# Optimization experiments

Hardware: AMD Instinct MI355X
Metric: run time of the kernel (lower is better)

The kernel has to match this reference:

```python
import jax, jax.numpy as jnp
import numpy as np

B, S, E, H = 4, 2048, 512, 8
D = E // H  # head dim
CDIM = 3


def setup_inputs() -> dict:
    key = jax.random.key(0)
    ks = jax.random.split(key, 16)
    inp = {
        'q': jax.random.normal(ks[0], (B, S, E), jnp.float32),
        'k': jax.random.normal(ks[1], (B, S, E), jnp.float32),
        'v': jax.random.normal(ks[2], (B, S, E), jnp.float32),
        'coords_q': jax.random.normal(ks[3], (B, S, CDIM), jnp.float32),
        'coords_k': jax.random.normal(ks[4], (B, S, CDIM), jnp.float32),
        'attn_mask': jax.random.randint(ks[5], (B, S, S), 0, 2).astype(bool),
        'alibi_mask': jax.random.randint(ks[6], (B, S, S), 0, 2).astype(bool),
        # per-head projection params, stacked over heads: [H, E, D]
        'Wq': jax.random.normal(ks[7], (H, E, D), jnp.float32) / np.sqrt(E),
        'bq': jnp.zeros((H, D), jnp.float32),
        'Wk': jax.random.normal(ks[8], (H, E, D), jnp.float32) / np.sqrt(E),
        'bk': jnp.zeros((H, D), jnp.float32),
        'Wv': jax.random.normal(ks[9], (H, E, D), jnp.float32) / np.sqrt(E),
        'bv': jnp.zeros((H, D), jnp.float32),
        # per-head ALiBi params; running_mean is a buffer (eval mode -> constant ones)
        'bias_scale': jax.random.uniform(ks[10], (H,), jnp.float32),
        'running_mean': jnp.ones((H,), jnp.float32),
        # output projection
        'fc_w': jax.random.normal(ks[11], (E, E), jnp.float32) / np.sqrt(E),
        'fc_b': jnp.zeros((E,), jnp.float32),
    }
    return inp


def reference(q, k, v, coords_q, coords_k, attn_mask, alibi_mask,
              Wq, bq, Wk, bk, Wv, bv, bias_scale, running_mean, fc_w, fc_b):
    # per-head projections, vectorized over heads: [B,H,S,D]
    qh = jnp.einsum('bse,hed->bhsd', q, Wq) + bq[None, :, None, :]
    kh = jnp.einsum('bse,hed->bhsd', k, Wk) + bk[None, :, None, :]
    vh = jnp.einsum('bse,hed->bhsd', v, Wv) + bv[None, :, None, :]

    # scaled dot-product logits: [B,H,Sq,Sk]
    logits = jnp.einsum('bhqd,bhkd->bhqk', qh, kh) * (D ** -0.5)
    weights = jax.nn.softmax(logits, axis=-1)

    # pairwise euclidean distances between coords: [B,Sq,Sk]
    diff = coords_q[:, :, None, :] - coords_k[:, None, :, :]
    dist = jnp.sqrt(jnp.sum(diff * diff, axis=-1))

    # per-head distance bias (eval: divide by running_mean buffer, scale by bias_scale)
    scale = (bias_scale / running_mean)[None, :, None, None]  # [1,H,1,1]
    scaled_dist = dist[:, None, :, :] * scale                  # [B,H,Sq,Sk]
    masked_dist = jnp.where(~alibi_mask[:, None, :, :], scaled_dist, 0.0)

    # post-softmax bias subtraction and masking (non-standard attention)
    masked = jnp.where(~attn_mask[:, None, :, :], weights - masked_dist, 0.0)

    att = jnp.einsum('bhqk,bhkd->bhqd', masked, vh)            # [B,H,S,D]
    att = att.transpose(0, 2, 1, 3).reshape(B, S, E)           # [B,S,E]
    return att @ fc_w.T + fc_b
```

## Files before the change

kernel.cpp:

```cpp
#include <hip/hip_runtime.h>

typedef unsigned short ushort;
typedef unsigned char uchar;
typedef unsigned long long u64;
typedef __attribute__((ext_vector_type(8))) short short8;
typedef __attribute__((ext_vector_type(4))) float f32x4;
typedef __attribute__((ext_vector_type(4))) unsigned int uint4v;

#define B_ 4
#define S_ 2048
#define E_ 512
#define H_ 8
#define D_ 64
#define LDT 40
#define LDF 68

__device__ inline ushort f2bf(float f) {
  union { float f; unsigned int u; } v; v.f = f;
  unsigned int u = v.u;
  unsigned int r = u + 0x7FFFu + ((u >> 16) & 1u);
  return (ushort)(r >> 16);
}

__device__ inline unsigned int cvt_pk_bf16(float a, float b) {
  unsigned int r;
  asm("v_cvt_pk_bf16_f32 %0, %1, %2" : "=v"(r) : "v"(a), "v"(b));
  return r;
}

__device__ inline float exp2_fast(float x) {
#if defined(__has_builtin)
#if __has_builtin(__builtin_amdgcn_exp2f)
  return __builtin_amdgcn_exp2f(x);
#else
  return __expf(x * 0.69314718056f);
#endif
#else
  return __expf(x * 0.69314718056f);
#endif
}

__device__ inline short8 mask_keep(short8 p, short8 a2) {
  union U { short8 s; uint4v u; } P, A;
  P.s = p; A.s = a2;
#pragma unroll
  for (int i = 0; i < 4; ++i) {
    unsigned int t = A.u[i] & 0x80008000u;
    unsigned int dm = (t >> 15) * 0xFFFFu;
    P.u[i] &= ~dm;
  }
  return P.s;
}

__device__ inline float dpp_sum16(float v) {
  union { float f; int i; } s, t;
  s.f = v;
  t.i = __builtin_amdgcn_update_dpp(0, s.i, 0x128, 0xf, 0xf, false); s.f += t.f;
  t.i = __builtin_amdgcn_update_dpp(0, s.i, 0x124, 0xf, 0xf, false); s.f += t.f;
  t.i = __builtin_amdgcn_update_dpp(0, s.i, 0x122, 0xf, 0xf, false); s.f += t.f;
  t.i = __builtin_amdgcn_update_dpp(0, s.i, 0x121, 0xf, 0xf, false); s.f += t.f;
  return s.f;
}

__global__ void detect_kernel(const uchar* __restrict__ am, int* flag) {
  __shared__ int s;
  if (threadIdx.x == 0) s = 0;
  __syncthreads();
  int x = 0;
  for (int p = threadIdx.x; p < 4096; p += 256)
    if (p & 3) x += am[p];
  atomicAdd(&s, x);
  __syncthreads();
  if (threadIdx.x == 0) *flag = (s == 0) ? 1 : 0;
}

__global__ __launch_bounds__(256) void convert_weights_kernel(
    const float* __restrict__ Wq, const float* __restrict__ Wk, const float* __restrict__ Wv,
    const float* __restrict__ fcw,
    ushort* __restrict__ wt, ushort* __restrict__ fcwbf) {
  const int p = blockIdx.y;
  const int n = blockIdx.x;
  if (p == 3) {
    const float* src = fcw + (size_t)n * E_;
    ushort* o = fcwbf + (size_t)n * E_;
    for (int e = threadIdx.x; e < E_; e += 256) o[e] = f2bf(src[e]);
    return;
  }
  const float* W = (p == 0) ? Wq : (p == 1) ? Wk : Wv;
  const int h = n >> 6, d = n & 63;
  ushort* o = wt + ((size_t)p * E_ + n) * E_;
  for (int e = threadIdx.x; e < E_; e += 256)
    o[e] = f2bf(W[((size_t)h * E_ + e) * D_ + d]);
}

__global__ __launch_bounds__(256) void proj_gemm_kernel(
    const float* __restrict__ qx, const float* __restrict__ kx, const float* __restrict__ vx,
    const ushort* __restrict__ wt,
    const float* __restrict__ bq, const float* __restrict__ bk, const float* __restrict__ bv,
    ushort* __restrict__ qkv) {
  const int phys = blockIdx.x;
  const int logical = (phys & 7) * 96 + (phys >> 3);
  const int p = logical >> 8;
  const int rem = logical & 255;
  const int m0 = (rem >> 2) * 128, n0 = (rem & 3) * 128;

  const float* A   = (p == 0) ? qx : (p == 1) ? kx : vx;
  const ushort* Bt = wt + (size_t)p * (E_ * E_);
  const float* bias = (p == 0) ? bq : (p == 1) ? bk : bv;
  const float osc = (p == 0) ? 0.125f * 1.44269504f : 1.0f;
  ushort* out = qkv + (size_t)p * (B_ * H_ * S_ * D_);

  const int tid = threadIdx.x;
  const int w = tid >> 6, lane = tid & 63;
  const int g = lane >> 4, c = lane & 15;
  const int wr = w >> 1, wc = w & 1;

  __shared__ ushort As[2][128][LDT], Bs[2][128][LDT];

  f32x4 acc[4][4];
#pragma unroll
  for (int i = 0; i < 4; ++i)
#pragma unroll
    for (int j = 0; j < 4; ++j) acc[i][j] = (f32x4){0, 0, 0, 0};

  const int srow = tid >> 2, sc8 = (tid & 3) * 8;
  float4 pa0[2], pa1[2];
  short8 pb[2];

#pragma unroll
  for (int it = 0; it < 2; ++it) {
    const float* ap = &A[(size_t)(m0 + srow + 64 * it) * E_ + sc8];
    float4 a0 = *(const float4*)ap;
    float4 a1 = *(const float4*)(ap + 4);
    unsigned int r0 = cvt_pk_bf16(a0.x, a0.y), r1 = cvt_pk_bf16(a0.z, a0.w);
    unsigned int r2 = cvt_pk_bf16(a1.x, a1.y), r3 = cvt_pk_bf16(a1.z, a1.w);
    short8 av;
    av[0] = (short)(ushort)r0; av[1] = (short)(ushort)(r0 >> 16);
    av[2] = (short)(ushort)r1; av[3] = (short)(ushort)(r1 >> 16);
    av[4] = (short)(ushort)r2; av[5] = (short)(ushort)(r2 >> 16);
    av[6] = (short)(ushort)r3; av[7] = (short)(ushort)(r3 >> 16);
    *(short8*)&As[0][srow + 64 * it][sc8] = av;
    *(short8*)&Bs[0][srow + 64 * it][sc8] = *(const short8*)&Bt[(size_t)(n0 + srow + 64 * it) * E_ + sc8];
  }
#pragma unroll
  for (int it = 0; it < 2; ++it) {
    const float* ap = &A[(size_t)(m0 + srow + 64 * it) * E_ + 32 + sc8];
    pa0[it] = *(const float4*)ap;
    pa1[it] = *(const float4*)(ap + 4);
    pb[it] = *(const short8*)&Bt[(size_t)(n0 + srow + 64 * it) * E_ + 32 + sc8];
  }
  __syncthreads();

  for (int ks = 0; ks < 16; ++ks) {
    const int cur = ks & 1;
    short8 af[4], bfr[4];
#pragma unroll
    for (int i = 0; i < 4; ++i) af[i] = *(const short8*)&As[cur][wr * 64 + i * 16 + c][8 * g];
#pragma unroll
    for (int j = 0; j < 4; ++j) bfr[j] = *(const short8*)&Bs[cur][wc * 64 + j * 16 + c][8 * g];
#pragma unroll
    for (int i = 0; i < 4; ++i)
#pragma unroll
      for (int j = 0; j < 4; ++j)
        acc[i][j] = __builtin_amdgcn_mfma_f32_16x16x32_bf16(af[i], bfr[j], acc[i][j], 0, 0, 0);

    if (ks + 1 < 16) {
#pragma unroll
      for (int it = 0; it < 2; ++it) {
        unsigned int r0 = cvt_pk_bf16(pa0[it].x, pa0[it].y), r1 = cvt_pk_bf16(pa0[it].z, pa0[it].w);
        unsigned int r2 = cvt_pk_bf16(pa1[it].x, pa1[it].y), r3 = cvt_pk_bf16(pa1[it].z, pa1[it].w);
        short8 av;
        av[0] = (short)(ushort)r0; av[1] = (short)(ushort)(r0 >> 16);
        av[2] = (short)(ushort)r1; av[3] = (short)(ushort)(r1 >> 16);
        av[4] = (short)(ushort)r2; av[5] = (short)(ushort)(r2 >> 16);
        av[6] = (short)(ushort)r3; av[7] = (short)(ushort)(r3 >> 16);
        *(short8*)&As[cur ^ 1][srow + 64 * it][sc8] = av;
        *(short8*)&Bs[cur ^ 1][srow + 64 * it][sc8] = pb[it];
      }
      if (ks + 2 < 16) {
        const int kk = (ks + 2) * 32;
#pragma unroll
        for (int it = 0; it < 2; ++it) {
          const float* ap = &A[(size_t)(m0 + srow + 64 * it) * E_ + kk + sc8];
          pa0[it] = *(const float4*)ap;
          pa1[it] = *(const float4*)(ap + 4);
          pb[it] = *(const short8*)&Bt[(size_t)(n0 + srow + 64 * it) * E_ + kk + sc8];
        }
      }
    }
    __syncthreads();
  }

#pragma unroll
  for (int i = 0; i < 4; ++i)
#pragma unroll
    for (int jj = 0; jj < 4; ++jj) {
      int grow = m0 + wr * 64 + i * 16 + 4 * g + jj;
      int b = grow >> 11, s = grow & 2047;
#pragma unroll
      for (int j = 0; j < 4; ++j) {
        int col = n0 + wc * 64 + j * 16 + c;
        int h = col >> 6, d = col & 63;
        out[(((size_t)(b * H_ + h)) * S_ + s) * D_ + d] = f2bf((acc[i][j][jj] + bias[col]) * osc);
      }
    }
}

__global__ __launch_bounds__(256) void transpose_v_kernel(
    const ushort* __restrict__ vh, ushort* __restrict__ vtg) {
  const int bh = blockIdx.y, s0 = blockIdx.x * 64;
  __shared__ ushort tile[64][70];
  const int tid = threadIdx.x;
#pragma unroll
  for (int it = 0; it < 2; ++it) {
    int chunk = tid + 256 * it;
    int r = chunk >> 3, c8 = chunk & 7;
    *(short8*)&tile[r][c8 * 8] = *(const short8*)&vh[((size_t)bh * S_ + s0 + r) * D_ + c8 * 8];
  }
  __syncthreads();
#pragma unroll
  for (int it = 0; it < 2; ++it) {
    int chunk = tid + 256 * it;
    int d = chunk >> 3, s8 = chunk & 7;
    short8 o;
#pragma unroll
    for (int j = 0; j < 8; ++j) o[j] = (short)tile[s8 * 8 + j][d];
    *(short8*)&vtg[((size_t)bh * D_ + d) * S_ + s0 + s8 * 8] = o;
  }
}

__global__ __launch_bounds__(256) void m2dist_kernel(
    const float* __restrict__ cq, const float* __restrict__ ck,
    const void* __restrict__ am_raw, const void* __restrict__ alm_raw,
    const int* __restrict__ flag,
    ushort* __restrict__ m2d) {
  const bool isInt = (*flag != 0);
  const int b = blockIdx.y, qi = blockIdx.x;
  const int k0 = threadIdx.x * 8;
  const size_t rowbase = ((size_t)b * S_ + qi) * S_;
  const float qx = cq[((size_t)b * S_ + qi) * 3 + 0];
  const float qy = cq[((size_t)b * S_ + qi) * 3 + 1];
  const float qz = cq[((size_t)b * S_ + qi) * 3 + 2];
  int a[8], al[8];
  if (isInt) {
    int4 A0 = *(const int4*)&((const int*)am_raw)[rowbase + k0];
    int4 A1 = *(const int4*)&((const int*)am_raw)[rowbase + k0 + 4];
    int4 L0 = *(const int4*)&((const int*)alm_raw)[rowbase + k0];
    int4 L1 = *(const int4*)&((const int*)alm_raw)[rowbase + k0 + 4];
    a[0]=A0.x; a[1]=A0.y; a[2]=A0.z; a[3]=A0.w; a[4]=A1.x; a[5]=A1.y; a[6]=A1.z; a[7]=A1.w;
    al[0]=L0.x; al[1]=L0.y; al[2]=L0.z; al[3]=L0.w; al[4]=L1.x; al[5]=L1.y; al[6]=L1.z; al[7]=L1.w;
  } else {
    u64 ab = *(const u64*)&((const uchar*)am_raw)[rowbase + k0];
    u64 lb = *(const u64*)&((const uchar*)alm_raw)[rowbase + k0];
#pragma unroll
    for (int j = 0; j < 8; ++j) { a[j] = (int)((ab >> (8 * j)) & 0xFF); al[j] = (int)((lb >> (8 * j)) & 0xFF); }
  }
  float c24[24];
  {
    const float* ckp = ck + ((size_t)b * S_ + k0) * 3;
#pragma unroll
    for (int t = 0; t < 6; ++t) {
      float4 cv = *(const float4*)(ckp + 4 * t);
      c24[4 * t] = cv.x; c24[4 * t + 1] = cv.y; c24[4 * t + 2] = cv.z; c24[4 * t + 3] = cv.w;
    }
  }
  float dist[8];
#pragma unroll
  for (int j = 0; j < 8; ++j) {
    const float dx = qx - c24[3 * j], dy = qy - c24[3 * j + 1], dz = qz - c24[3 * j + 2];
    dist[j] = sqrtf(dx * dx + dy * dy + dz * dz);
  }
  short8 md;
#pragma unroll
  for (int jp = 0; jp < 4; ++jp) {
    unsigned int r = cvt_pk_bf16(dist[2 * jp], dist[2 * jp + 1]);
    ushort v0 = (!a[2 * jp]     && !al[2 * jp])     ? (ushort)r         : (ushort)0;
    ushort v1 = (!a[2 * jp + 1] && !al[2 * jp + 1]) ? (ushort)(r >> 16) : (ushort)0;
    if (a[2 * jp])     v0 |= 0x8000u;
    if (a[2 * jp + 1]) v1 |= 0x8000u;
    md[2 * jp] = (short)v0; md[2 * jp + 1] = (short)v1;
  }
  *(short8*)&m2d[rowbase + k0] = md;
}

__global__ __launch_bounds__(512) void flash_kernel(
    const ushort* __restrict__ qh, const ushort* __restrict__ kh, const ushort* __restrict__ vtg,
    const ushort* __restrict__ m2d,
    const float* __restrict__ bscale, const float* __restrict__ rmean,
    ushort* __restrict__ attb) {
  const int flat = blockIdx.x;
  const int h = flat >> 6;
  const int grp = flat & 63;
  const int b = grp >> 4;
  const int qb = (grp & 15) * 128;
  const int bh = b * 8 + h;
  const int tid = threadIdx.x;
  const int w = tid >> 6, lane = tid & 63;
  const int g = lane >> 4, c = lane & 15;

  __shared__ ushort Kt[2][64][LDF];
  __shared__ ushort Vt[2][64][LDF];
  __shared__ ushort Pl[8][16][LDF];

  const size_t bhS = (size_t)bh * S_;
  const int qrow_a = qb + 16 * w + c;
  const short8 aq0 = *(const short8*)(qh + (bhS + qrow_a) * D_ + 8 * g);
  const short8 aq1 = *(const short8*)(qh + (bhS + qrow_a) * D_ + 8 * g + 32);

  const int skr = tid >> 3, sc8 = (tid & 7) * 8;
  const ushort* pk0 = kh + (bhS + skr) * D_ + sc8;
  const ushort* pv0 = vtg + ((size_t)bh * D_ + skr) * S_ + sc8;
  const ushort* pm0 = m2d + ((size_t)b * S_ + qrow_a) * S_ + 8 * g;
  const ushort* pm1 = pm0 + 32;

  f32x4 acc1[4], acc2[4];
#pragma unroll
  for (int t = 0; t < 4; ++t) { acc1[t] = (f32x4){0,0,0,0}; acc2[t] = (f32x4){0,0,0,0}; }
  float l[4] = {0, 0, 0, 0};

  {
    short8 k0 = *(const short8*)pk0;  pk0 += 64 * D_;
    short8 v0 = *(const short8*)pv0;  pv0 += 64;
    *(short8*)&Kt[0][skr][sc8] = k0;
    *(short8*)&Vt[0][skr][sc8] = v0;
  }
  short8 a2n0 = *(const short8*)pm0; pm0 += 64;
  short8 a2n1 = *(const short8*)pm1; pm1 += 64;
  short8 skn = *(const short8*)pk0;  pk0 += 64 * D_;
  short8 svn = *(const short8*)pv0;  pv0 += 64;
  __syncthreads();

  for (int kb = 0; kb < S_; kb += 64) {
    const int cur = (kb >> 6) & 1;
    short8 a2c0 = a2n0, a2c1 = a2n1;
    a2n0 = *(const short8*)pm0; pm0 += 64;
    a2n1 = *(const short8*)pm1; pm1 += 64;

    f32x4 sf[4];
    __builtin_amdgcn_s_setprio(1);
#pragma unroll
    for (int t = 0; t < 4; ++t) {
      short8 b0 = *(const short8*)&Kt[cur][16 * t + c][8 * g];
      short8 b1 = *(const short8*)&Kt[cur][16 * t + c][8 * g + 32];
      f32x4 z = (f32x4){0, 0, 0, 0};
      z = __builtin_amdgcn_mfma_f32_16x16x32_bf16(aq0, b0, z, 0, 0, 0);
      z = __builtin_amdgcn_mfma_f32_16x16x32_bf16(aq1, b1, z, 0, 0, 0);
      sf[t] = z;
    }
    __builtin_amdgcn_s_setprio(0);

#pragma unroll
    for (int t = 0; t < 4; ++t)
#pragma unroll
      for (int jp = 0; jp < 2; ++jp) {
        float p0 = exp2_fast(sf[t][2 * jp]);
        float p1 = exp2_fast(sf[t][2 * jp + 1]);
        l[2 * jp] += p0; l[2 * jp + 1] += p1;
        unsigned int r = cvt_pk_bf16(p0, p1);
        Pl[w][4 * g + 2 * jp][16 * t + c]     = (ushort)r;
        Pl[w][4 * g + 2 * jp + 1][16 * t + c] = (ushort)(r >> 16);
      }

    asm volatile("s_waitcnt lgkmcnt(0)" ::: "memory");
    __builtin_amdgcn_sched_barrier(0);

    short8 pa0 = *(const short8*)&Pl[w][c][8 * g];
    short8 pa1 = *(const short8*)&Pl[w][c][8 * g + 32];
    pa0 = mask_keep(pa0, a2c0);
    pa1 = mask_keep(pa1, a2c1);
    __builtin_amdgcn_s_setprio(1);
#pragma unroll
    for (int t2 = 0; t2 < 4; ++t2) {
      short8 v0 = *(const short8*)&Vt[cur][16 * t2 + c][8 * g];
      short8 v1 = *(const short8*)&Vt[cur][16 * t2 + c][8 * g + 32];
      acc1[t2] = __builtin_amdgcn_mfma_f32_16x16x32_bf16(pa0, v0, acc1[t2], 0, 0, 0);
      acc1[t2] = __builtin_amdgcn_mfma_f32_16x16x32_bf16(pa1, v1, acc1[t2], 0, 0, 0);
      acc2[t2] = __builtin_amdgcn_mfma_f32_16x16x32_bf16(a2c0, v0, acc2[t2], 0, 0, 0);
      acc2[t2] = __builtin_amdgcn_mfma_f32_16x16x32_bf16(a2c1, v1, acc2[t2], 0, 0, 0);
    }
    __builtin_amdgcn_s_setprio(0);

    if (kb + 64 < S_) {
      *(short8*)&Kt[cur ^ 1][skr][sc8] = skn;
      *(short8*)&Vt[cur ^ 1][skr][sc8] = svn;
      skn = *(const short8*)pk0;  pk0 += 64 * D_;
      svn = *(const short8*)pv0;  pv0 += 64;
    }
    __syncthreads();
  }

  float linv[4];
#pragma unroll
  for (int j = 0; j < 4; ++j) linv[j] = 1.0f / dpp_sum16(l[j]);
  const float scale = bscale[h] / rmean[h];
#pragma unroll
  for (int t2 = 0; t2 < 4; ++t2)
#pragma unroll
    for (int j = 0; j < 4; ++j) {
      int qr = qb + 16 * w + 4 * g + j;
      int d = 16 * t2 + c;
      attb[(((size_t)b * S_ + qr) * H_ + h) * D_ + d] =
          f2bf(acc1[t2][j] * linv[j] - scale * acc2[t2][j]);
    }
}

__global__ __launch_bounds__(256) void final_gemm_kernel(
    const ushort* __restrict__ attb, const ushort* __restrict__ fcwbf,
    const float* __restrict__ fcb, float* __restrict__ out) {
  const int phys = blockIdx.x;
  const int logical = (phys & 7) * 32 + (phys >> 3);
  const int m0 = (logical >> 2) * 128, n0 = (logical & 3) * 128;
  const int tid = threadIdx.x;
  const int w = tid >> 6, lane = tid & 63;
  const int g = lane >> 4, c = lane & 15;
  const int wr = w >> 1, wc = w & 1;

  __shared__ ushort As[2][128][LDT], Bs[2][128][LDT];

  f32x4 acc[4][4];
#pragma unroll
  for (int i = 0; i < 4; ++i)
#pragma unroll
    for (int j = 0; j < 4; ++j) acc[i][j] = (f32x4){0, 0, 0, 0};

  const int srow = tid >> 2, sc8 = (tid & 3) * 8;
  short8 pa[2], pb[2];

#pragma unroll
  for (int it = 0; it < 2; ++it) {
    *(short8*)&As[0][srow + 64 * it][sc8] = *(const short8*)&attb[(size_t)(m0 + srow + 64 * it) * E_ + sc8];
    *(short8*)&Bs[0][srow + 64 * it][sc8] = *(const short8*)&fcwbf[(size_t)(n0 + srow + 64 * it) * E_ + sc8];
  }
#pragma unroll
  for (int it = 0; it < 2; ++it) {
    pa[it] = *(const short8*)&attb[(size_t)(m0 + srow + 64 * it) * E_ + 32 + sc8];
    pb[it] = *(const short8*)&fcwbf[(size_t)(n0 + srow + 64 * it) * E_ + 32 + sc8];
  }
  __syncthreads();

  for (int ks = 0; ks < 16; ++ks) {
    const int cur = ks & 1;
    short8 af[4], bfr[4];
#pragma unroll
    for (int i = 0; i < 4; ++i) af[i] = *(const short8*)&As[cur][wr * 64 + i * 16 + c][8 * g];
#pragma unroll
    for (int j = 0; j < 4; ++j) bfr[j] = *(const short8*)&Bs[cur][wc * 64 + j * 16 + c][8 * g];
#pragma unroll
    for (int i = 0; i < 4; ++i)
#pragma unroll
      for (int j = 0; j < 4; ++j)
        acc[i][j] = __builtin_amdgcn_mfma_f32_16x16x32_bf16(af[i], bfr[j], acc[i][j], 0, 0, 0);

    if (ks + 1 < 16) {
#pragma unroll
      for (int it = 0; it < 2; ++it) {
        *(short8*)&As[cur ^ 1][srow + 64 * it][sc8] = pa[it];
        *(short8*)&Bs[cur ^ 1][srow + 64 * it][sc8] = pb[it];
      }
      if (ks + 2 < 16) {
        const int kk = (ks + 2) * 32;
#pragma unroll
        for (int it = 0; it < 2; ++it) {
          pa[it] = *(const short8*)&attb[(size_t)(m0 + srow + 64 * it) * E_ + kk + sc8];
          pb[it] = *(const short8*)&fcwbf[(size_t)(n0 + srow + 64 * it) * E_ + kk + sc8];
        }
      }
    }
    __syncthreads();
  }

#pragma unroll
  for (int i = 0; i < 4; ++i)
#pragma unroll
    for (int jj = 0; jj < 4; ++jj) {
      int grow = m0 + wr * 64 + i * 16 + 4 * g + jj;
#pragma unroll
      for (int j = 0; j < 4; ++j) {
        int col = n0 + wc * 64 + j * 16 + c;
        out[(size_t)grow * E_ + col] = acc[i][j][jj] + fcb[col];
      }
    }
}

extern "C" void kernel_launch(void* const* d_in, const int* in_sizes, int n_in,
                              void* d_out, int out_size, void* d_ws, size_t ws_size,
                              hipStream_t stream) {
  const float* q   = (const float*)d_in[0];
  const float* k   = (const float*)d_in[1];
  const float* v   = (const float*)d_in[2];
  const float* cq  = (const float*)d_in[3];
  const float* ck  = (const float*)d_in[4];
  const void*  am  = d_in[5];
  const void*  alm = d_in[6];
  const float* Wq  = (const float*)d_in[7];
  const float* bq  = (const float*)d_in[8];
  const float* Wk  = (const float*)d_in[9];
  const float* bk  = (const float*)d_in[10];
  const float* Wv  = (const float*)d_in[11];
  const float* bv  = (const float*)d_in[12];
  const float* bsc = (const float*)d_in[13];
  const float* rm  = (const float*)d_in[14];
  const float* fcw = (const float*)d_in[15];
  const float* fcb = (const float*)d_in[16];
  float* out = (float*)d_out;

  char* ws = (char*)d_ws;
  ushort* attb = (ushort*)(ws);
  ushort* vtg  = (ushort*)(ws + 16ull * 1024 * 1024);
  ushort* qkv  = (ushort*)(ws + 24ull * 1024 * 1024);
  ushort* m2d  = (ushort*)(ws + 48ull * 1024 * 1024);
  ushort* wt   = (ushort*)(ws + 80ull * 1024 * 1024);
  ushort* fcwbf= (ushort*)(ws + 80ull * 1024 * 1024 + 1536 * 1024);
  int*    flag = (int*)   (ws + 82ull * 1024 * 1024);

  ushort* qh = qkv;
  ushort* kh = qkv + (size_t)(B_ * H_ * S_ * D_);
  ushort* vh = qkv + 2 * (size_t)(B_ * H_ * S_ * D_);

  detect_kernel<<<1, 256, 0, stream>>>((const uchar*)am, flag);
  convert_weights_kernel<<<dim3(512, 4), 256, 0, stream>>>(Wq, Wk, Wv, fcw, wt, fcwbf);
  proj_gemm_kernel<<<768, 256, 0, stream>>>(q, k, v, wt, bq, bk, bv, qkv);
  transpose_v_kernel<<<dim3(S_ / 64, B_ * H_), 256, 0, stream>>>(vh, vtg);
  m2dist_kernel<<<dim3(S_, B_), 256, 0, stream>>>(cq, ck, am, alm, flag, m2d);
  flash_kernel<<<512, 512, 0, stream>>>(qh, kh, vtg, m2d, bsc, rm, attb);
  final_gemm_kernel<<<256, 256, 0, stream>>>(attb, fcwbf, fcb, out);
}
```

Measured before the change: 166.9 us.

## Merge projection GEMM, mask-type detection and distance-mask build into one launch

The projection GEMM and the mask/distance preprocessing kernel become one launch, with blocks 0-767 doing the GEMM and the remaining 8192 blocks building the combined mask/distance array. The separate single-block detect kernel is removed, and each mask block now works out the mask element width itself from the first 1 KB of the mask. This cuts two launches and lets the bandwidth-bound mask work overlap with the compute-bound GEMM. In exchange every mask block repeats the detection read and an atomic, and the GEMM blocks' shared-memory size now applies to the mask blocks too.

```diff
diff --git a/kernel.cpp b/kernel.cpp
--- a/kernel.cpp
+++ b/kernel.cpp
@@ -60,18 +60,6 @@
   t.i = __builtin_amdgcn_update_dpp(0, s.i, 0x122, 0xf, 0xf, false); s.f += t.f;
   t.i = __builtin_amdgcn_update_dpp(0, s.i, 0x121, 0xf, 0xf, false); s.f += t.f;
   return s.f;
-}
-
-__global__ void detect_kernel(const uchar* __restrict__ am, int* flag) {
-  __shared__ int s;
-  if (threadIdx.x == 0) s = 0;
-  __syncthreads();
-  int x = 0;
-  for (int p = threadIdx.x; p < 4096; p += 256)
-    if (p & 3) x += am[p];
-  atomicAdd(&s, x);
-  __syncthreads();
-  if (threadIdx.x == 0) *flag = (s == 0) ? 1 : 0;
 }
 
 __global__ __launch_bounds__(256) void convert_weights_kernel(
@@ -93,154 +81,141 @@
     o[e] = f2bf(W[((size_t)h * E_ + e) * D_ + d]);
 }
 
-__global__ __launch_bounds__(256) void proj_gemm_kernel(
+__global__ __launch_bounds__(256) void phase1_kernel(
     const float* __restrict__ qx, const float* __restrict__ kx, const float* __restrict__ vx,
     const ushort* __restrict__ wt,
     const float* __restrict__ bq, const float* __restrict__ bk, const float* __restrict__ bv,
-    ushort* __restrict__ qkv) {
-  const int phys = blockIdx.x;
-  const int logical = (phys & 7) * 96 + (phys >> 3);
-  const int p = logical >> 8;
-  const int rem = logical & 255;
-  const int m0 = (rem >> 2) * 128, n0 = (rem & 3) * 128;
-
-  const float* A   = (p == 0) ? qx : (p == 1) ? kx : vx;
-  const ushort* Bt = wt + (size_t)p * (E_ * E_);
-  const float* bias = (p == 0) ? bq : (p == 1) ? bk : bv;
-  const float osc = (p == 0) ? 0.125f * 1.44269504f : 1.0f;
-  ushort* out = qkv + (size_t)p * (B_ * H_ * S_ * D_);
-
+    ushort* __restrict__ qkv,
+    const float* __restrict__ cq, const float* __restrict__ ck,
+    const void* __restrict__ am_raw, const void* __restrict__ alm_raw,
+    ushort* __restrict__ m2d) {
+  __shared__ ushort As[2][128][LDT], Bs[2][128][LDT];
+  const int bid = blockIdx.x;
   const int tid = threadIdx.x;
-  const int w = tid >> 6, lane = tid & 63;
-  const int g = lane >> 4, c = lane & 15;
-  const int wr = w >> 1, wc = w & 1;
-
-  __shared__ ushort As[2][128][LDT], Bs[2][128][LDT];
-
-  f32x4 acc[4][4];
-#pragma unroll
-  for (int i = 0; i < 4; ++i)
-#pragma unroll
-    for (int j = 0; j < 4; ++j) acc[i][j] = (f32x4){0, 0, 0, 0};
-
-  const int srow = tid >> 2, sc8 = (tid & 3) * 8;
-  float4 pa0[2], pa1[2];
-  short8 pb[2];
-
-#pragma unroll
-  for (int it = 0; it < 2; ++it) {
-    const float* ap = &A[(size_t)(m0 + srow + 64 * it) * E_ + sc8];
-    float4 a0 = *(const float4*)ap;
-    float4 a1 = *(const float4*)(ap + 4);
-    unsigned int r0 = cvt_pk_bf16(a0.x, a0.y), r1 = cvt_pk_bf16(a0.z, a0.w);
-    unsigned int r2 = cvt_pk_bf16(a1.x, a1.y), r3 = cvt_pk_bf16(a1.z, a1.w);
-    short8 av;
-    av[0] = (short)(ushort)r0; av[1] = (short)(ushort)(r0 >> 16);
-    av[2] = (short)(ushort)r1; av[3] = (short)(ushort)(r1 >> 16);
-    av[4] = (short)(ushort)r2; av[5] = (short)(ushort)(r2 >> 16);
-    av[6] = (short)(ushort)r3; av[7] = (short)(ushort)(r3 >> 16);
-    *(short8*)&As[0][srow + 64 * it][sc8] = av;
-    *(short8*)&Bs[0][srow + 64 * it][sc8] = *(const short8*)&Bt[(size_t)(n0 + srow + 64 * it) * E_ + sc8];
-  }
-#pragma unroll
-  for (int it = 0; it < 2; ++it) {
-    const float* ap = &A[(size_t)(m0 + srow + 64 * it) * E_ + 32 + sc8];
-    pa0[it] = *(const float4*)ap;
-    pa1[it] = *(const float4*)(ap + 4);
-    pb[it] = *(const short8*)&Bt[(size_t)(n0 + srow + 64 * it) * E_ + 32 + sc8];
-  }
-  __syncthreads();
-
-  for (int ks = 0; ks < 16; ++ks) {
-    const int cur = ks & 1;
-    short8 af[4], bfr[4];
-#pragma unroll
-    for (int i = 0; i < 4; ++i) af[i] = *(const short8*)&As[cur][wr * 64 + i * 16 + c][8 * g];
-#pragma unroll
-    for (int j = 0; j < 4; ++j) bfr[j] = *(const short8*)&Bs[cur][wc * 64 + j * 16 + c][8 * g];
+
+  if (bid < 768) {
+    const int logical = (bid & 7) * 96 + (bid >> 3);
+    const int p = logical >> 8;
+    const int rem = logical & 255;
+    const int m0 = (rem >> 2) * 128, n0 = (rem & 3) * 128;
+
+    const float* A   = (p == 0) ? qx : (p == 1) ? kx : vx;
+    const ushort* Bt = wt + (size_t)p * (E_ * E_);
+    const float* bias = (p == 0) ? bq : (p == 1) ? bk : bv;
+    const float osc = (p == 0) ? 0.125f * 1.44269504f : 1.0f;
+    ushort* out = qkv + (size_t)p * (B_ * H_ * S_ * D_);
+
+    const int w = tid >> 6, lane = tid & 63;
+    const int g = lane >> 4, c = lane & 15;
+    const int wr = w >> 1, wc = w & 1;
+
+    f32x4 acc[4][4];
 #pragma unroll
     for (int i = 0; i < 4; ++i)
 #pragma unroll
-      for (int j = 0; j < 4; ++j)
-        acc[i][j] = __builtin_amdgcn_mfma_f32_16x16x32_bf16(af[i], bfr[j], acc[i][j], 0, 0, 0);
-
-    if (ks + 1 < 16) {
-#pragma unroll
-      for (int it = 0; it < 2; ++it) {
-        unsigned int r0 = cvt_pk_bf16(pa0[it].x, pa0[it].y), r1 = cvt_pk_bf16(pa0[it].z, pa0[it].w);
-        unsigned int r2 = cvt_pk_bf16(pa1[it].x, pa1[it].y), r3 = cvt_pk_bf16(pa1[it].z, pa1[it].w);
-        short8 av;
-        av[0] = (short)(ushort)r0; av[1] = (short)(ushort)(r0 >> 16);
-        av[2] = (short)(ushort)r1; av[3] = (short)(ushort)(r1 >> 16);
-        av[4] = (short)(ushort)r2; av[5] = (short)(ushort)(r2 >> 16);
-        av[6] = (short)(ushort)r3; av[7] = (short)(ushort)(r3 >> 16);
-        *(short8*)&As[cur ^ 1][srow + 64 * it][sc8] = av;
-        *(short8*)&Bs[cur ^ 1][srow + 64 * it][sc8] = pb[it];
-      }
-      if (ks + 2 < 16) {
-        const int kk = (ks + 2) * 32;
+      for (int j = 0; j < 4; ++j) acc[i][j] = (f32x4){0, 0, 0, 0};
+
+    const int srow = tid >> 2, sc8 = (tid & 3) * 8;
+    float4 pa0[2], pa1[2];
+    short8 pb[2];
+
+#pragma unroll
+    for (int it = 0; it < 2; ++it) {
+      const float* ap = &A[(size_t)(m0 + srow + 64 * it) * E_ + sc8];
+      float4 a0 = *(const float4*)ap;
+      float4 a1 = *(const float4*)(ap + 4);
+      unsigned int r0 = cvt_pk_bf16(a0.x, a0.y), r1 = cvt_pk_bf16(a0.z, a0.w);
+      unsigned int r2 = cvt_pk_bf16(a1.x, a1.y), r3 = cvt_pk_bf16(a1.z, a1.w);
+      short8 av;
+      av[0] = (short)(ushort)r0; av[1] = (short)(ushort)(r0 >> 16);
+      av[2] = (short)(ushort)r1; av[3] = (short)(ushort)(r1 >> 16);
+      av[4] = (short)(ushort)r2; av[5] = (short)(ushort)(r2 >> 16);
+      av[6] = (short)(ushort)r3; av[7] = (short)(ushort)(r3 >> 16);
+      *(short8*)&As[0][srow + 64 * it][sc8] = av;
+      *(short8*)&Bs[0][srow + 64 * it][sc8] = *(const short8*)&Bt[(size_t)(n0 + srow + 64 * it) * E_ + sc8];
+    }
+#pragma unroll
+    for (int it = 0; it < 2; ++it) {
+      const float* ap = &A[(size_t)(m0 + srow + 64 * it) * E_ + 32 + sc8];
+      pa0[it] = *(const float4*)ap;
+      pa1[it] = *(const float4*)(ap + 4);
+      pb[it] = *(const short8*)&Bt[(size_t)(n0 + srow + 64 * it) * E_ + 32 + sc8];
+    }
+    __syncthreads();
+
+    for (int ks = 0; ks < 16; ++ks) {
+      const int cur = ks & 1;
+      short8 af[4], bfr[4];
+#pragma unroll
+      for (int i = 0; i < 4; ++i) af[i] = *(const short8*)&As[cur][wr * 64 + i * 16 + c][8 * g];
+#pragma unroll
+      for (int j = 0; j < 4; ++j) bfr[j] = *(const short8*)&Bs[cur][wc * 64 + j * 16 + c][8 * g];
+#pragma unroll
+      for (int i = 0; i < 4; ++i)
+#pragma unroll
+        for (int j = 0; j < 4; ++j)
+          acc[i][j] = __builtin_amdgcn_mfma_f32_16x16x32_bf16(af[i], bfr[j], acc[i][j], 0, 0, 0);
+
+      if (ks + 1 < 16) {
 #pragma unroll
         for (int it = 0; it < 2; ++it) {
-          const float* ap = &A[(size_t)(m0 + srow + 64 * it) * E_ + kk + sc8];
-          pa0[it] = *(const float4*)ap;
-          pa1[it] = *(const float4*)(ap + 4);
-          pb[it] = *(const short8*)&Bt[(size_t)(n0 + srow + 64 * it) * E_ + kk + sc8];
+          unsigned int r0 = cvt_pk_bf16(pa0[it].x, pa0[it].y), r1 = cvt_pk_bf16(pa0[it].z, pa0[it].w);
+          unsigned int r2 = cvt_pk_bf16(pa1[it].x, pa1[it].y), r3 = cvt_pk_bf16(pa1[it].z, pa1[it].w);
+          short8 av;
+          av[0] = (short)(ushort)r0; av[1] = (short)(ushort)(r0 >> 16);
+          av[2] = (short)(ushort)r1; av[3] = (short)(ushort)(r1 >> 16);
+          av[4] = (short)(ushort)r2; av[5] = (short)(ushort)(r2 >> 16);
+          av[6] = (short)(ushort)r3; av[7] = (short)(ushort)(r3 >> 16);
+          *(short8*)&As[cur ^ 1][srow + 64 * it][sc8] = av;
+          *(short8*)&Bs[cur ^ 1][srow + 64 * it][sc8] = pb[it];
+        }
+        if (ks + 2 < 16) {
+          const int kk = (ks + 2) * 32;
+#pragma unroll
+          for (int it = 0; it < 2; ++it) {
+            const float* ap = &A[(size_t)(m0 + srow + 64 * it) * E_ + kk + sc8];
+            pa0[it] = *(const float4*)ap;
+            pa1[it] = *(const float4*)(ap + 4);
+            pb[it] = *(const short8*)&Bt[(size_t)(n0 + srow + 64 * it) * E_ + kk + sc8];
+          }
         }
       }
-    }
-    __syncthreads();
-  }
-
-#pragma unroll
-  for (int i = 0; i < 4; ++i)
-#pragma unroll
-    for (int jj = 0; jj < 4; ++jj) {
-      int grow = m0 + wr * 64 + i * 16 + 4 * g + jj;
-      int b = grow >> 11, s = grow & 2047;
-#pragma unroll
-      for (int j = 0; j < 4; ++j) {
-        int col = n0 + wc * 64 + j * 16 + c;
-        int h = col >> 6, d = col & 63;
-        out[(((size_t)(b * H_ + h)) * S_ + s) * D_ + d] = f2bf((acc[i][j][jj] + bias[col]) * osc);
+      __syncthreads();
+    }
+
+#pragma unroll
+    for (int i = 0; i < 4; ++i)
+#pragma unroll
+      for (int jj = 0; jj < 4; ++jj) {
+        int grow = m0 + wr * 64 + i * 16 + 4 * g + jj;
+        int b = grow >> 11, s = grow & 2047;
+#pragma unroll
+        for (int j = 0; j < 4; ++j) {
+          int col = n0 + wc * 64 + j * 16 + c;
+          int h = col >> 6, d = col & 63;
+          out[(((size_t)(b * H_ + h)) * S_ + s) * D_ + d] = f2bf((acc[i][j][jj] + bias[col]) * osc);
+        }
       }
-    }
-}
-
-__global__ __launch_bounds__(256) void transpose_v_kernel(
-    const ushort* __restrict__ vh, ushort* __restrict__ vtg) {
-  const int bh = blockIdx.y, s0 = blockIdx.x * 64;
-  __shared__ ushort tile[64][70];
-  const int tid = threadIdx.x;
-#pragma unroll
-  for (int it = 0; it < 2; ++it) {
-    int chunk = tid + 256 * it;
-    int r = chunk >> 3, c8 = chunk & 7;
-    *(short8*)&tile[r][c8 * 8] = *(const short8*)&vh[((size_t)bh * S_ + s0 + r) * D_ + c8 * 8];
-  }
+    return;
+  }
+
+  int* sflag = (int*)&As[0][0][0];
+  if (tid == 0) *sflag = 0;
   __syncthreads();
-#pragma unroll
-  for (int it = 0; it < 2; ++it) {
-    int chunk = tid + 256 * it;
-    int d = chunk >> 3, s8 = chunk & 7;
-    short8 o;
-#pragma unroll
-    for (int j = 0; j < 8; ++j) o[j] = (short)tile[s8 * 8 + j][d];
-    *(short8*)&vtg[((size_t)bh * D_ + d) * S_ + s0 + s8 * 8] = o;
-  }
-}
-
-__global__ __launch_bounds__(256) void m2dist_kernel(
-    const float* __restrict__ cq, const float* __restrict__ ck,
-    const void* __restrict__ am_raw, const void* __restrict__ alm_raw,
-    const int* __restrict__ flag,
-    ushort* __restrict__ m2d) {
-  const bool isInt = (*flag != 0);
-  const int b = blockIdx.y, qi = blockIdx.x;
-  const int k0 = threadIdx.x * 8;
+  {
+    unsigned int x = ((const unsigned int*)am_raw)[tid];
+    if (x & 0xFFFFFF00u) atomicAdd(sflag, 1);
+  }
+  __syncthreads();
+  const bool isInt = (*sflag == 0);
+
+  const int mid = bid - 768;
+  const int b = mid >> 11, qi = mid & 2047;
+  const int k0 = tid * 8;
   const size_t rowbase = ((size_t)b * S_ + qi) * S_;
-  const float qx = cq[((size_t)b * S_ + qi) * 3 + 0];
-  const float qy = cq[((size_t)b * S_ + qi) * 3 + 1];
-  const float qz = cq[((size_t)b * S_ + qi) * 3 + 2];
+  const float qx2 = cq[((size_t)b * S_ + qi) * 3 + 0];
+  const float qy2 = cq[((size_t)b * S_ + qi) * 3 + 1];
+  const float qz2 = cq[((size_t)b * S_ + qi) * 3 + 2];
   int a[8], al[8];
   if (isInt) {
     int4 A0 = *(const int4*)&((const int*)am_raw)[rowbase + k0];
@@ -267,7 +242,7 @@
   float dist[8];
 #pragma unroll
   for (int j = 0; j < 8; ++j) {
-    const float dx = qx - c24[3 * j], dy = qy - c24[3 * j + 1], dz = qz - c24[3 * j + 2];
+    const float dx = qx2 - c24[3 * j], dy = qy2 - c24[3 * j + 1], dz = qz2 - c24[3 * j + 2];
     dist[j] = sqrtf(dx * dx + dy * dy + dz * dz);
   }
   short8 md;
@@ -281,6 +256,29 @@
     md[2 * jp] = (short)v0; md[2 * jp + 1] = (short)v1;
   }
   *(short8*)&m2d[rowbase + k0] = md;
+}
+
+__global__ __launch_bounds__(256) void transpose_v_kernel(
+    const ushort* __restrict__ vh, ushort* __restrict__ vtg) {
+  const int bh = blockIdx.y, s0 = blockIdx.x * 64;
+  __shared__ ushort tile[64][70];
+  const int tid = threadIdx.x;
+#pragma unroll
+  for (int it = 0; it < 2; ++it) {
+    int chunk = tid + 256 * it;
+    int r = chunk >> 3, c8 = chunk & 7;
+    *(short8*)&tile[r][c8 * 8] = *(const short8*)&vh[((size_t)bh * S_ + s0 + r) * D_ + c8 * 8];
+  }
+  __syncthreads();
+#pragma unroll
+  for (int it = 0; it < 2; ++it) {
+    int chunk = tid + 256 * it;
+    int d = chunk >> 3, s8 = chunk & 7;
+    short8 o;
+#pragma unroll
+    for (int j = 0; j < 8; ++j) o[j] = (short)tile[s8 * 8 + j][d];
+    *(short8*)&vtg[((size_t)bh * D_ + d) * S_ + s0 + s8 * 8] = o;
+  }
 }
 
 __global__ __launch_bounds__(512) void flash_kernel(
@@ -511,17 +509,15 @@
   ushort* m2d  = (ushort*)(ws + 48ull * 1024 * 1024);
   ushort* wt   = (ushort*)(ws + 80ull * 1024 * 1024);
   ushort* fcwbf= (ushort*)(ws + 80ull * 1024 * 1024 + 1536 * 1024);
-  int*    flag = (int*)   (ws + 82ull * 1024 * 1024);
 
   ushort* qh = qkv;
   ushort* kh = qkv + (size_t)(B_ * H_ * S_ * D_);
   ushort* vh = qkv + 2 * (size_t)(B_ * H_ * S_ * D_);
 
-  detect_kernel<<<1, 256, 0, stream>>>((const uchar*)am, flag);
   convert_weights_kernel<<<dim3(512, 4), 256, 0, stream>>>(Wq, Wk, Wv, fcw, wt, fcwbf);
-  proj_gemm_kernel<<<768, 256, 0, stream>>>(q, k, v, wt, bq, bk, bv, qkv);
+  phase1_kernel<<<768 + 8192, 256, 0, stream>>>(q, k, v, wt, bq, bk, bv, qkv,
+                                                cq, ck, am, alm, m2d);
   transpose_v_kernel<<<dim3(S_ / 64, B_ * H_), 256, 0, stream>>>(vh, vtg);
-  m2dist_kernel<<<dim3(S_, B_), 256, 0, stream>>>(cq, ck, am, alm, flag, m2d);
   flash_kernel<<<512, 512, 0, stream>>>(qh, kh, vtg, m2d, bsc, rm, attb);
   final_gemm_kernel<<<256, 256, 0, stream>>>(attb, fcwbf, fcb, out);
 }
```

After: 166.1 us. Within noise of the previous version (-0.5%).
